# Performance work log

Hardware: AMD Instinct MI355X
Metric: run time of the kernel (lower is better)

Reference implementation:

```python
import jax, jax.numpy as jnp
import numpy as np
from jax import lax

NSTEPS = 4
STEPSIZE = 0.1


def setup_inputs() -> dict:
    key = jax.random.key(0)
    k1, k2, k3, k4 = jax.random.split(key, 4)
    B, N, D = 8, 40962, 40  # batch, n_patch, d_latent+d_ancillary
    H, D_DYN = 512, 32
    x = jax.random.normal(k1, (B, N, D), dtype=jnp.float32)
    # stencil: self + 3 neighbours per dual-mesh vertex
    nbrs = jax.random.randint(k2, (N, 3), 0, N, dtype=jnp.int32)
    index = jnp.concatenate([jnp.arange(N, dtype=jnp.int32)[:, None], nbrs], axis=1)  # (N,4)
    W1 = jax.random.normal(k3, (4, D, H), dtype=jnp.float32) * (1.0 / np.sqrt(4 * D))
    b1 = jnp.zeros((H,), dtype=jnp.float32)
    W2 = jax.random.normal(k4, (H, D_DYN), dtype=jnp.float32) * (1.0 / np.sqrt(H))
    b2 = jnp.zeros((D_DYN,), dtype=jnp.float32)
    return {"x": x, "index": index, "W1": W1, "b1": b1, "W2": W2, "b2": b2}


def interaction_model(z, W1, b1, W2, b2):
    # z: (B, N, 4, D) -> (B, N, d_dyn); MLP over flattened 4-vertex stencil
    h = jax.nn.gelu(jnp.einsum('bnkd,kdh->bnh', z, W1) + b1)
    return h @ W2 + b2


def reference(x, index, W1, b1, W2, b2):
    D = x.shape[-1]
    d_dyn = W2.shape[-1]

    def step(x, _):
        z = x[:, index, :]                       # (B, N, 4, D) gather of 4-neighbour stencil
        fz = interaction_model(z, W1, b1, W2, b2)  # (B, N, d_dyn)
        dx = jnp.pad(fz, ((0, 0), (0, 0), (0, D - d_dyn)))  # ancillary channels untouched
        return x + STEPSIZE * dx, None

    x, _ = lax.scan(step, x, None, length=NSTEPS)
    return x
```

## Files before the change

kernel.cpp:

```cpp
#include <hip/hip_runtime.h>
#include <math.h>

constexpr int BB   = 8;
constexpr int NN   = 40962;
constexpr int DDIM = 40;
constexpr int HH   = 512;
constexpr int DDYN = 32;
constexpr float STEPSZ = 0.1f;

constexpr int TM   = 32;
constexpr int NTHR = 512;
constexpr int ZS   = 168;

constexpr size_t X_ELEMS = (size_t)BB * NN * DDIM;
constexpr size_t X_BYTES = X_ELEMS * 4;
constexpr int W1P_ELEMS = 32 * 5 * 64 * 8;
constexpr int W2P_BYTES = 2 * 16 * 64 * 8;

constexpr int Z_BYTES = TM * ZS * 2;
constexpr int H_OFF   = Z_BYTES;
constexpr int LDS_TOT = Z_BYTES + TM * HH;

typedef __attribute__((ext_vector_type(8))) short short8;
typedef __attribute__((ext_vector_type(4))) float f32x4;
typedef __attribute__((ext_vector_type(4))) unsigned short u16x4;

__device__ __forceinline__ unsigned short bf16_rne(float f) {
    unsigned int u = __float_as_uint(f);
    return (unsigned short)((u + 0x7FFFu + ((u >> 16) & 1u)) >> 16);
}

__device__ __forceinline__ unsigned char f32_to_fp8_sw(float f) {
    if (!(f == f)) return 0x7f;
    unsigned u = __float_as_uint(f);
    unsigned s = (u >> 24) & 0x80u;
    float a = fabsf(f);
    if (a >= 464.f) return (unsigned char)(s | 0x7e);
    int e = (int)((u >> 23) & 0xff) - 127;
    if (e < -6) {
        int q = (int)fminf(fmaxf(a * 512.0f + 0.5f, 0.f), 7.f);
        return (unsigned char)(s | q);
    }
    unsigned m = u & 0x7fffffu;
    unsigned keep = m >> 20, rest = m & 0xfffffu;
    keep += (rest > 0x80000u || (rest == 0x80000u && (keep & 1u))) ? 1u : 0u;
    if (keep == 8u) { keep = 0u; ++e; if (e > 8) return (unsigned char)(s | 0x7e); }
    return (unsigned char)(s | ((unsigned)(e + 7) << 3) | keep);
}

__device__ __forceinline__ unsigned int pk4_fp8(float a, float b, float c, float d) {
#if __has_builtin(__builtin_amdgcn_cvt_pk_fp8_f32)
    int r = __builtin_amdgcn_cvt_pk_fp8_f32(a, b, 0, false);
    r     = __builtin_amdgcn_cvt_pk_fp8_f32(c, d, r, true);
    return (unsigned int)r;
#else
    return (unsigned)f32_to_fp8_sw(a) | ((unsigned)f32_to_fp8_sw(b) << 8) |
           ((unsigned)f32_to_fp8_sw(c) << 16) | ((unsigned)f32_to_fp8_sw(d) << 24);
#endif
}

__device__ __forceinline__ float gelu_fast(float x) {
    float u = x * fmaf(0.044715f, x * x, 1.0f);
    float e = __expf(-1.5957691216057308f * u);
    return x * __builtin_amdgcn_rcpf(1.0f + e);
}

__global__ __launch_bounds__(256) void pack_w1(const float* __restrict__ W1,
                                               unsigned short* __restrict__ W1p) {
    int t = blockIdx.x * 256 + threadIdx.x;
    if (t >= W1P_ELEMS) return;
    int j = t & 7, ln = (t >> 3) & 63, g = t >> 9;
    int kk = g % 5, mt = g / 5;
    int nl = ln & 15, q = ln >> 4;
    int k = kk * 32 + q * 8 + j, m = mt * 16 + nl;
    W1p[t] = bf16_rne(W1[(size_t)k * HH + m]);
}
__global__ __launch_bounds__(256) void pack_w2_fp8(const float* __restrict__ W2,
                                                   unsigned char* __restrict__ W2p) {
    int t = blockIdx.x * 256 + threadIdx.x;
    if (t >= W2P_BYTES) return;
    int j = t & 7, ln = (t >> 3) & 63, g = t >> 9;
    int kk = g & 15, jt = g >> 4;
    int nl = ln & 15, q = ln >> 4;
    int k = kk * 32 + q * 8 + j, m = jt * 16 + nl;
    float v = W2[(size_t)k * DDYN + m];
#if __has_builtin(__builtin_amdgcn_cvt_pk_fp8_f32)
    W2p[t] = (unsigned char)(__builtin_amdgcn_cvt_pk_fp8_f32(v, v, 0, false) & 0xff);
#else
    W2p[t] = f32_to_fp8_sw(v);
#endif
}

__global__ __launch_bounds__(NTHR, 6) void step_mfma(
    const float* __restrict__ xsrc, float* __restrict__ xdst,
    const int* __restrict__ index,
    const unsigned short* __restrict__ W1p, const float* __restrict__ b1,
    const unsigned char* __restrict__ W2p, const float* __restrict__ b2)
{
    __shared__ alignas(16) unsigned char smem[LDS_TOT];
    unsigned short* z = (unsigned short*)smem;
    unsigned char*  h = smem + H_OFF;
    float* fz0 = (float*)smem;
    float* fz1 = (float*)(smem + TM * 36 * 4);

    const int tid = threadIdx.x;
    const int w   = tid >> 6;
    const int ln  = tid & 63;
    const int nl  = ln & 15;
    const int q   = ln >> 4;
    const int n0  = blockIdx.x * TM;
    const int b   = blockIdx.y;
    const size_t xbase = (size_t)b * NN * DDIM;

    for (int e = tid; e < TM * 4 * 10; e += NTHR) {
        int m = e / 40, r = e - m * 40;
        int k = r / 10, qq = r - k * 10;
        u16x4 out = (u16x4)0;
        int n = n0 + m;
        if (n < NN) {
            int nb = index[n * 4 + k];
            float4 v = ((const float4*)(xsrc + xbase + (size_t)nb * DDIM))[qq];
            out.x = bf16_rne(v.x); out.y = bf16_rne(v.y);
            out.z = bf16_rne(v.z); out.w = bf16_rne(v.w);
        }
        *(u16x4*)(z + m * ZS + k * 40 + qq * 4) = out;
    }
    __syncthreads();

    f32x4 acc[4][2];
    #pragma unroll
    for (int i = 0; i < 4; ++i) {
        float4 bv = *(const float4*)(b1 + (w * 4 + i) * 16 + q * 4);
        f32x4 a; a[0] = bv.x; a[1] = bv.y; a[2] = bv.z; a[3] = bv.w;
        acc[i][0] = a; acc[i][1] = a;
    }
    #pragma unroll
    for (int kk = 0; kk < 5; ++kk) {
        short8 bfr[2];
        #pragma unroll
        for (int nt = 0; nt < 2; ++nt)
            bfr[nt] = *(const short8*)(z + (nt * 16 + nl) * ZS + kk * 32 + q * 8);
        #pragma unroll
        for (int i = 0; i < 4; ++i) {
            short8 afr = *(const short8*)(W1p + (size_t)(((w * 4 + i) * 5 + kk) * 512 + ln * 8));
            #pragma unroll
            for (int nt = 0; nt < 2; ++nt)
                acc[i][nt] = __builtin_amdgcn_mfma_f32_16x16x32_bf16(afr, bfr[nt], acc[i][nt], 0, 0, 0);
        }
    }
    __syncthreads();

    #pragma unroll
    for (int i = 0; i < 4; ++i) {
        const int hid  = (w * 4 + i) * 16 + q * 4;
        const int sub8 = hid >> 3;
        const int o4   = (q & 1) << 2;
        #pragma unroll
        for (int nt = 0; nt < 2; ++nt) {
            f32x4 a = acc[i][nt];
            unsigned int p = pk4_fp8(gelu_fast(a[0]), gelu_fast(a[1]),
                                     gelu_fast(a[2]), gelu_fast(a[3]));
            int node = nt * 16 + nl;
            *(unsigned int*)(h + node * 512 + ((sub8 ^ (node & 7)) << 3) + o4) = p;
        }
    }
    __syncthreads();

    const int kh  = w >> 2;
    const int jt  = (w >> 1) & 1;
    const int nt2 = w & 1;
    const int hrow = nt2 * 16 + nl;
    f32x4 acc2;
    if (kh == 0) {
        float4 bv = *(const float4*)(b2 + jt * 16 + q * 4);
        acc2[0] = bv.x; acc2[1] = bv.y; acc2[2] = bv.z; acc2[3] = bv.w;
    } else {
        acc2[0] = acc2[1] = acc2[2] = acc2[3] = 0.f;
    }
    #pragma unroll
    for (int kk = 0; kk < 8; ++kk) {
        int kg = kh * 8 + kk;
        long long afr, bfr;
        __builtin_memcpy(&afr, W2p + (size_t)(((jt * 16 + kg) * 64 + ln) * 8), 8);
        __builtin_memcpy(&bfr, h + hrow * 512 + (((kg * 4 + q) ^ (hrow & 7)) << 3), 8);
        acc2 = __builtin_amdgcn_mfma_f32_16x16x32_fp8_fp8(afr, bfr, acc2, 0, 0, 0);
    }
    {
        float* fzk = kh ? fz1 : fz0;
        *(f32x4*)(fzk + hrow * 36 + jt * 16 + q * 4) = acc2;
    }
    __syncthreads();

    if (tid < TM * 10) {
        int m = tid / 10, p = tid - m * 10;
        int n = n0 + m;
        if (n < NN) {
            size_t off = xbase + (size_t)n * DDIM + p * 4;
            float4 v = *(const float4*)(xsrc + off);
            if (p < 8) {
                f32x4 f0 = *(const f32x4*)(fz0 + m * 36 + p * 4);
                f32x4 f1 = *(const f32x4*)(fz1 + m * 36 + p * 4);
                v.x = fmaf(STEPSZ, f0[0] + f1[0], v.x);
                v.y = fmaf(STEPSZ, f0[1] + f1[1], v.y);
                v.z = fmaf(STEPSZ, f0[2] + f1[2], v.z);
                v.w = fmaf(STEPSZ, f0[3] + f1[3], v.w);
            }
            *(float4*)(xdst + off) = v;
        }
    }
}

constexpr int FTM = 16;
__device__ __forceinline__ float gelu_f(float x) { return gelu_fast(x); }
__global__ __launch_bounds__(256) void step_f32(
    const float* __restrict__ xsrc, float* __restrict__ xdst,
    const int* __restrict__ index,
    const float* __restrict__ W1, const float* __restrict__ b1,
    const float* __restrict__ W2, const float* __restrict__ b2)
{
    __shared__ float z_lds[FTM][160];
    __shared__ float h_lds[FTM][HH];
    __shared__ float fz_lds[FTM][DDYN];
    const int tid = threadIdx.x, tile = blockIdx.x, b = blockIdx.y;
    const int n0 = tile * FTM;
    const int nvalid = min(FTM, NN - n0);
    for (int e = tid; e < FTM * 4 * 10; e += 256) {
        int m = e / 40, r = e % 40, k = r / 10, qq = r % 10;
        float4 v = make_float4(0.f, 0.f, 0.f, 0.f);
        int n = n0 + m;
        if (n < NN) {
            int nb = index[n * 4 + k];
            v = ((const float4*)(xsrc + ((size_t)b * NN + nb) * DDIM))[qq];
        }
        ((float4*)&z_lds[m][k * DDIM])[qq] = v;
    }
    __syncthreads();
    const int c0 = 2 * tid;
    float2 acc[FTM];
    {
        float bx = b1[c0], by = b1[c0 + 1];
        #pragma unroll
        for (int m = 0; m < FTM; ++m) { acc[m].x = bx; acc[m].y = by; }
    }
    for (int kd = 0; kd < 160; kd += 4) {
        float2 w0 = *(const float2*)(W1 + (size_t)(kd + 0) * HH + c0);
        float2 w1 = *(const float2*)(W1 + (size_t)(kd + 1) * HH + c0);
        float2 w2 = *(const float2*)(W1 + (size_t)(kd + 2) * HH + c0);
        float2 w3 = *(const float2*)(W1 + (size_t)(kd + 3) * HH + c0);
        #pragma unroll
        for (int m = 0; m < FTM; ++m) {
            float4 zv = *(const float4*)&z_lds[m][kd];
            acc[m].x = fmaf(zv.x, w0.x, acc[m].x); acc[m].y = fmaf(zv.x, w0.y, acc[m].y);
            acc[m].x = fmaf(zv.y, w1.x, acc[m].x); acc[m].y = fmaf(zv.y, w1.y, acc[m].y);
            acc[m].x = fmaf(zv.z, w2.x, acc[m].x); acc[m].y = fmaf(zv.z, w2.y, acc[m].y);
            acc[m].x = fmaf(zv.w, w3.x, acc[m].x); acc[m].y = fmaf(zv.w, w3.y, acc[m].y);
        }
    }
    #pragma unroll
    for (int m = 0; m < FTM; ++m) {
        h_lds[m][c0]     = gelu_f(acc[m].x);
        h_lds[m][c0 + 1] = gelu_f(acc[m].y);
    }
    __syncthreads();
    {
        const int j = tid & 31, mg = tid >> 5;
        float a0 = b2[j], a1 = a0;
        for (int c = 0; c < HH; c += 4) {
            float wa = W2[(size_t)(c + 0) * DDYN + j];
            float wb = W2[(size_t)(c + 1) * DDYN + j];
            float wc = W2[(size_t)(c + 2) * DDYN + j];
            float wd = W2[(size_t)(c + 3) * DDYN + j];
            float4 h0 = *(const float4*)&h_lds[mg][c];
            float4 h1 = *(const float4*)&h_lds[mg + 8][c];
            a0 = fmaf(h0.x, wa, a0); a0 = fmaf(h0.y, wb, a0);
            a0 = fmaf(h0.z, wc, a0); a0 = fmaf(h0.w, wd, a0);
            a1 = fmaf(h1.x, wa, a1); a1 = fmaf(h1.y, wb, a1);
            a1 = fmaf(h1.z, wc, a1); a1 = fmaf(h1.w, wd, a1);
        }
        fz_lds[mg][j] = a0; fz_lds[mg + 8][j] = a1;
    }
    __syncthreads();
    const size_t base = ((size_t)b * NN + n0) * (size_t)DDIM;
    for (int e = tid; e < nvalid * DDIM; e += 256) {
        int m = e / DDIM, d = e % DDIM;
        float v = xsrc[base + e];
        if (d < DDYN) v = fmaf(STEPSZ, fz_lds[m][d], v);
        xdst[base + e] = v;
    }
}

extern "C" void kernel_launch(void* const* d_in, const int* in_sizes, int n_in,
                              void* d_out, int out_size, void* d_ws, size_t ws_size,
                              hipStream_t stream) {
    const float* x   = (const float*)d_in[0];
    const int*   idx = (const int*)  d_in[1];
    const float* W1  = (const float*)d_in[2];
    const float* b1  = (const float*)d_in[3];
    const float* W2  = (const float*)d_in[4];
    const float* b2  = (const float*)d_in[5];
    float* out  = (float*)d_out;
    float* xbuf = (float*)d_ws;

    const size_t need = X_BYTES + (size_t)W1P_ELEMS * 2 + W2P_BYTES;
    if (ws_size >= need) {
        unsigned short* W1p = (unsigned short*)((char*)d_ws + X_BYTES);
        unsigned char*  W2p = (unsigned char*)(W1p + W1P_ELEMS);
        pack_w1<<<(W1P_ELEMS + 255) / 256, 256, 0, stream>>>(W1, W1p);
        pack_w2_fp8<<<(W2P_BYTES + 255) / 256, 256, 0, stream>>>(W2, W2p);
        dim3 grid((NN + TM - 1) / TM, BB), block(NTHR);
        step_mfma<<<grid, block, 0, stream>>>(x,    xbuf, idx, W1p, b1, W2p, b2);
        step_mfma<<<grid, block, 0, stream>>>(xbuf, out,  idx, W1p, b1, W2p, b2);
        step_mfma<<<grid, block, 0, stream>>>(out,  xbuf, idx, W1p, b1, W2p, b2);
        step_mfma<<<grid, block, 0, stream>>>(xbuf, out,  idx, W1p, b1, W2p, b2);
    } else {
        dim3 grid((NN + FTM - 1) / FTM, BB), block(256);
        step_f32<<<grid, block, 0, stream>>>(x,    xbuf, idx, W1, b1, W2, b2);
        step_f32<<<grid, block, 0, stream>>>(xbuf, out,  idx, W1, b1, W2, b2);
        step_f32<<<grid, block, 0, stream>>>(out,  xbuf, idx, W1, b1, W2, b2);
        step_f32<<<grid, block, 0, stream>>>(xbuf, out,  idx, W1, b1, W2, b2);
    }
}
```

Baseline: 664.2 us.

## Double node tile to 64 with 1024 threads, cache self rows in LDS

Raises the node tile from 32 to 64 and the block size from 512 to 1024 threads, and remaps the warps so each loads two W1 fragments and reuses them across four node subtiles. This cuts W1 global reads per node. It also stashes each node's own x row in LDS during the gather so the final residual update does not reload it from global memory. Smaller changes swap software bf16 rounding for the hardware packed convert and use a raw v_exp_f32 in GELU. The trade-off is higher LDS use and larger blocks, which may lower occupancy, and the self-row capture assumes index[n,0]==n.

```diff
diff --git a/kernel.cpp b/kernel.cpp
--- a/kernel.cpp
+++ b/kernel.cpp
@@ -8,8 +8,8 @@
 constexpr int DDYN = 32;
 constexpr float STEPSZ = 0.1f;
 
-constexpr int TM   = 32;
-constexpr int NTHR = 512;
+constexpr int TM   = 64;
+constexpr int NTHR = 1024;
 constexpr int ZS   = 168;
 
 constexpr size_t X_ELEMS = (size_t)BB * NN * DDIM;
@@ -19,7 +19,9 @@
 
 constexpr int Z_BYTES = TM * ZS * 2;
 constexpr int H_OFF   = Z_BYTES;
-constexpr int LDS_TOT = Z_BYTES + TM * HH;
+constexpr int H_BYTES = TM * HH;
+constexpr int XS_OFF  = H_OFF + H_BYTES;
+constexpr int LDS_TOT = XS_OFF + TM * DDIM * 4;
 
 typedef __attribute__((ext_vector_type(8))) short short8;
 typedef __attribute__((ext_vector_type(4))) float f32x4;
@@ -28,6 +30,18 @@
 __device__ __forceinline__ unsigned short bf16_rne(float f) {
     unsigned int u = __float_as_uint(f);
     return (unsigned short)((u + 0x7FFFu + ((u >> 16) & 1u)) >> 16);
+}
+
+__device__ __forceinline__ unsigned int cvt_pk_bf16(float lo, float hi) {
+    unsigned int r;
+    asm("v_cvt_pk_bf16_f32 %0, %1, %2" : "=v"(r) : "v"(lo), "v"(hi));
+    return r;
+}
+
+__device__ __forceinline__ float exp2_hw(float x) {
+    float r;
+    asm("v_exp_f32 %0, %1" : "=v"(r) : "v"(x));
+    return r;
 }
 
 __device__ __forceinline__ unsigned char f32_to_fp8_sw(float f) {
@@ -61,7 +75,7 @@
 
 __device__ __forceinline__ float gelu_fast(float x) {
     float u = x * fmaf(0.044715f, x * x, 1.0f);
-    float e = __expf(-1.5957691216057308f * u);
+    float e = exp2_hw(-2.30220817f * u);
     return x * __builtin_amdgcn_rcpf(1.0f + e);
 }
 
@@ -91,7 +105,7 @@
 #endif
 }
 
-__global__ __launch_bounds__(NTHR, 6) void step_mfma(
+__global__ __launch_bounds__(NTHR, 8) void step_mfma(
     const float* __restrict__ xsrc, float* __restrict__ xdst,
     const int* __restrict__ index,
     const unsigned short* __restrict__ W1p, const float* __restrict__ b1,
@@ -100,6 +114,7 @@
     __shared__ alignas(16) unsigned char smem[LDS_TOT];
     unsigned short* z = (unsigned short*)smem;
     unsigned char*  h = smem + H_OFF;
+    float* xself = (float*)(smem + XS_OFF);
     float* fz0 = (float*)smem;
     float* fz1 = (float*)(smem + TM * 36 * 4);
 
@@ -115,48 +130,47 @@
     for (int e = tid; e < TM * 4 * 10; e += NTHR) {
         int m = e / 40, r = e - m * 40;
         int k = r / 10, qq = r - k * 10;
-        u16x4 out = (u16x4)0;
+        unsigned int lo = 0, hi = 0;
         int n = n0 + m;
         if (n < NN) {
             int nb = index[n * 4 + k];
             float4 v = ((const float4*)(xsrc + xbase + (size_t)nb * DDIM))[qq];
-            out.x = bf16_rne(v.x); out.y = bf16_rne(v.y);
-            out.z = bf16_rne(v.z); out.w = bf16_rne(v.w);
-        }
-        *(u16x4*)(z + m * ZS + k * 40 + qq * 4) = out;
-    }
-    __syncthreads();
-
-    f32x4 acc[4][2];
-    #pragma unroll
-    for (int i = 0; i < 4; ++i) {
-        float4 bv = *(const float4*)(b1 + (w * 4 + i) * 16 + q * 4);
+            lo = cvt_pk_bf16(v.x, v.y);
+            hi = cvt_pk_bf16(v.z, v.w);
+            if (k == 0) *(float4*)(xself + m * 40 + qq * 4) = v;
+        }
+        *(uint2*)(z + m * ZS + k * 40 + qq * 4) = make_uint2(lo, hi);
+    }
+    __syncthreads();
+
+    f32x4 acc[2][4];
+    #pragma unroll
+    for (int i = 0; i < 2; ++i) {
+        float4 bv = *(const float4*)(b1 + (w * 2 + i) * 16 + q * 4);
         f32x4 a; a[0] = bv.x; a[1] = bv.y; a[2] = bv.z; a[3] = bv.w;
-        acc[i][0] = a; acc[i][1] = a;
+        #pragma unroll
+        for (int nt = 0; nt < 4; ++nt) acc[i][nt] = a;
     }
     #pragma unroll
     for (int kk = 0; kk < 5; ++kk) {
-        short8 bfr[2];
-        #pragma unroll
-        for (int nt = 0; nt < 2; ++nt)
-            bfr[nt] = *(const short8*)(z + (nt * 16 + nl) * ZS + kk * 32 + q * 8);
-        #pragma unroll
-        for (int i = 0; i < 4; ++i) {
-            short8 afr = *(const short8*)(W1p + (size_t)(((w * 4 + i) * 5 + kk) * 512 + ln * 8));
-            #pragma unroll
-            for (int nt = 0; nt < 2; ++nt)
-                acc[i][nt] = __builtin_amdgcn_mfma_f32_16x16x32_bf16(afr, bfr[nt], acc[i][nt], 0, 0, 0);
-        }
-    }
-    __syncthreads();
-
-    #pragma unroll
-    for (int i = 0; i < 4; ++i) {
-        const int hid  = (w * 4 + i) * 16 + q * 4;
+        short8 afr0 = *(const short8*)(W1p + (size_t)(((w * 2 + 0) * 5 + kk) * 512 + ln * 8));
+        short8 afr1 = *(const short8*)(W1p + (size_t)(((w * 2 + 1) * 5 + kk) * 512 + ln * 8));
+        #pragma unroll
+        for (int nt = 0; nt < 4; ++nt) {
+            short8 bfr = *(const short8*)(z + (nt * 16 + nl) * ZS + kk * 32 + q * 8);
+            acc[0][nt] = __builtin_amdgcn_mfma_f32_16x16x32_bf16(afr0, bfr, acc[0][nt], 0, 0, 0);
+            acc[1][nt] = __builtin_amdgcn_mfma_f32_16x16x32_bf16(afr1, bfr, acc[1][nt], 0, 0, 0);
+        }
+    }
+    __syncthreads();
+
+    #pragma unroll
+    for (int i = 0; i < 2; ++i) {
+        const int hid  = (w * 2 + i) * 16 + q * 4;
         const int sub8 = hid >> 3;
         const int o4   = (q & 1) << 2;
         #pragma unroll
-        for (int nt = 0; nt < 2; ++nt) {
+        for (int nt = 0; nt < 4; ++nt) {
             f32x4 a = acc[i][nt];
             unsigned int p = pk4_fp8(gelu_fast(a[0]), gelu_fast(a[1]),
                                      gelu_fast(a[2]), gelu_fast(a[3]));
@@ -166,9 +180,9 @@
     }
     __syncthreads();
 
-    const int kh  = w >> 2;
-    const int jt  = (w >> 1) & 1;
-    const int nt2 = w & 1;
+    const int nt2 = w & 3;
+    const int jt  = (w >> 2) & 1;
+    const int kh  = (w >> 3) & 1;
     const int hrow = nt2 * 16 + nl;
     f32x4 acc2;
     if (kh == 0) {
@@ -195,8 +209,7 @@
         int m = tid / 10, p = tid - m * 10;
         int n = n0 + m;
         if (n < NN) {
-            size_t off = xbase + (size_t)n * DDIM + p * 4;
-            float4 v = *(const float4*)(xsrc + off);
+            float4 v = *(const float4*)(xself + m * 40 + p * 4);
             if (p < 8) {
                 f32x4 f0 = *(const f32x4*)(fz0 + m * 36 + p * 4);
                 f32x4 f1 = *(const f32x4*)(fz1 + m * 36 + p * 4);
@@ -205,7 +218,7 @@
                 v.z = fmaf(STEPSZ, f0[2] + f1[2], v.z);
                 v.w = fmaf(STEPSZ, f0[3] + f1[3], v.w);
             }
-            *(float4*)(xdst + off) = v;
+            *(float4*)(xdst + xbase + (size_t)n * DDIM + p * 4) = v;
         }
     }
 }
```

After: 647.1 us. 2.6% less time.
